# Kernel optimization log

Hardware: AMD Instinct MI355X
Metric: run time of the kernel (lower is better)

The kernel has to match this reference:

```python
import jax, jax.numpy as jnp
import numpy as np

B, V, C, D, H, W = 2, 5, 32, 32, 128, 160


def _grid_sample(img, grid):
    # img: [B,C,H,W]; grid: [B,Hg,Wg,2] in [-1,1]; bilinear, zeros padding, align_corners=True
    Bi, Ci, Hi, Wi = img.shape
    x = (grid[..., 0] + 1.0) * 0.5 * (Wi - 1)
    y = (grid[..., 1] + 1.0) * 0.5 * (Hi - 1)
    x0 = jnp.floor(x); y0 = jnp.floor(y)
    wx = x - x0; wy = y - y0

    def tap(im, ix, iy):
        valid = ((ix >= 0) & (ix <= Wi - 1) & (iy >= 0) & (iy <= Hi - 1)).astype(im.dtype)
        ixc = jnp.clip(ix, 0, Wi - 1).astype(jnp.int32)
        iyc = jnp.clip(iy, 0, Hi - 1).astype(jnp.int32)
        return im[:, iyc, ixc] * valid[None]  # [C,Hg,Wg]

    def one(im, x0b, y0b, wxb, wyb):
        v00 = tap(im, x0b, y0b); v01 = tap(im, x0b + 1, y0b)
        v10 = tap(im, x0b, y0b + 1); v11 = tap(im, x0b + 1, y0b + 1)
        return (v00 * (1 - wxb) + v01 * wxb) * (1 - wyb) + (v10 * (1 - wxb) + v11 * wxb) * wyb

    return jax.vmap(one)(img, x0, y0, wx, wy)


def _homo_warp(src_fea, src_proj, ref_proj, depth_values):
    # src_fea [B,C,H,W], projs [B,4,4], depth_values [B,D,H,W] -> [B,C,D,H,W]
    Bi, Ci, Hi, Wi = src_fea.shape
    Di = depth_values.shape[1]
    proj = src_proj @ jnp.linalg.inv(ref_proj)
    rot, trans = proj[:, :3, :3], proj[:, :3, 3]
    yy, xx = jnp.meshgrid(jnp.arange(Hi, dtype=src_fea.dtype), jnp.arange(Wi, dtype=src_fea.dtype), indexing='ij')
    xyz = jnp.stack([xx.ravel(), yy.ravel(), jnp.ones(Hi * Wi, src_fea.dtype)], 0)  # [3,HW]
    rot_xyz = jnp.einsum('bij,jn->bin', rot, xyz)  # [B,3,HW]
    pxyz = rot_xyz[:, :, None, :] * depth_values.reshape(Bi, 1, Di, Hi * Wi) + trans[:, :, None, None]
    z = pxyz[:, 2]
    gx = (pxyz[:, 0] / z) / ((Wi - 1) / 2) - 1
    gy = (pxyz[:, 1] / z) / ((Hi - 1) / 2) - 1
    grid = jax.lax.stop_gradient(jnp.stack([gx, gy], -1).reshape(Bi, Di * Hi, Wi, 2))  # torch.no_grad block
    return _grid_sample(src_fea, grid).reshape(Bi, Ci, Di, Hi, Wi)


def _pixelwise_net(vol, w0, b0, w1, b1, w2, b2):
    # vol [B,1,D,H,W]; 1x1x1 conv stack + sigmoid + max over depth -> [B,1,H,W]
    x = jax.nn.relu(jnp.einsum('oi,bidhw->bodhw', w0, vol) + b0[None, :, None, None, None])
    x = jax.nn.relu(jnp.einsum('oi,bidhw->bodhw', w1, x) + b1[None, :, None, None, None])
    x = jnp.einsum('oi,bidhw->bodhw', w2, x) + b2[None, :, None, None, None]
    return jnp.max(jax.nn.sigmoid(x), axis=2)


def _cost_reg(vol, w, b):
    out = jax.lax.conv_general_dilated(vol, w, (1, 1, 1), 'SAME', dimension_numbers=('NCDHW', 'OIDHW', 'NCDHW'))
    return out + b[None, :, None, None, None]


def _proj_new(pm):  # pm [B,2,4,4] -> [B,4,4]: K[:3,:3] @ E[:3,:4] into rows 0..2
    top = jnp.einsum('bij,bjk->bik', pm[:, 1, :3, :3], pm[:, 0, :3, :4])
    return pm[:, 0].at[:, :3, :4].set(top)


def _forward(features, proj_matrices, depth_values, pw_w0, pw_b0, pw_w1, pw_b1, pw_w2, pw_b2, reg_w, reg_b):
    proj_new = jax.vmap(_proj_new, in_axes=1, out_axes=1)(proj_matrices)  # [B,V,4,4]
    ref_fea = features[0]
    vol_sum = jnp.zeros((B, 1, D, H, W), features.dtype)  # torch broadcasts [B,1,...] into [B,C,...]; channels identical
    wsum = jnp.full((B, 1, 1, H, W), 1e-5, features.dtype)
    weights = []
    for v in range(1, V):
        warped = _homo_warp(features[v], proj_new[:, v], proj_new[:, 0], depth_values)  # [B,C,D,H,W]
        wvol = jnp.mean(warped * ref_fea[:, :, None], axis=1, keepdims=True)            # [B,1,D,H,W]
        vw = _pixelwise_net(wvol, pw_w0, pw_b0, pw_w1, pw_b1, pw_w2, pw_b2)             # [B,1,H,W]
        weights.append(vw)
        vol_sum = vol_sum + wvol * vw[:, :, None]
        wsum = wsum + vw[:, :, None]
    similarity = jnp.broadcast_to(vol_sum / wsum, (B, C, D, H, W))  # matches torch broadcast-into-C-channel volume
    prob_pre = _cost_reg(similarity, reg_w, reg_b)[:, 0]  # squeeze(1) -> [B,D,H,W]
    prob = jax.nn.softmax(prob_pre, axis=1)
    view_weights = jnp.concatenate(weights, axis=1)  # [B,V-1,H,W]
    idx = jnp.argmax(prob, axis=1, keepdims=True)
    depth = jnp.take_along_axis(depth_values, idx, axis=1)[:, 0]  # WTA depth [B,H,W]
    conf = jnp.max(prob, axis=1)
    return depth, conf, prob, view_weights


def setup_inputs() -> dict:
    key = jax.random.key(0)
    ks = jax.random.split(key, 8)
    features = jax.random.normal(ks[0], (V, B, C, H, W), jnp.float32)
    # Realistic projection matrices: [:,v,0]=extrinsics, [:,v,1,:3,:3]=intrinsics
    Kmat = np.eye(4, dtype=np.float32)
    Kmat[0, 0] = Kmat[1, 1] = 200.0
    Kmat[0, 2] = W / 2.0; Kmat[1, 2] = H / 2.0
    projs = np.zeros((B, V, 2, 4, 4), np.float32)
    for v in range(V):
        E = np.eye(4, dtype=np.float32)
        E[0, 3] = 10.0 * v; E[1, 3] = -5.0 * v  # small baselines
        projs[:, v, 0] = E
        projs[:, v, 1] = Kmat
    proj_matrices = jnp.asarray(projs)
    dv = jnp.linspace(425.0, 935.0, D, dtype=jnp.float32)
    depth_values = jnp.broadcast_to(dv[None, :, None, None], (B, D, H, W))
    def init(k, shape, fan):
        return jax.random.normal(k, shape, jnp.float32) / np.sqrt(fan)
    return {
        'features': features,
        'proj_matrices': proj_matrices,
        'depth_values': depth_values,
        'pw_w0': init(ks[1], (16, 1), 1), 'pw_b0': jnp.zeros(16, jnp.float32),
        'pw_w1': init(ks[2], (8, 16), 16), 'pw_b1': jnp.zeros(8, jnp.float32),
        'pw_w2': init(ks[3], (1, 8), 8), 'pw_b2': jnp.zeros(1, jnp.float32),
        'reg_w': init(ks[4], (1, C, 3, 3, 3), C * 27), 'reg_b': jnp.zeros(1, jnp.float32),
    }


def reference(features, proj_matrices, depth_values, pw_w0, pw_b0, pw_w1, pw_b1, pw_w2, pw_b2, reg_w, reg_b):
    return _forward(features, proj_matrices, depth_values, pw_w0, pw_b0, pw_w1, pw_b1, pw_w2, pw_b2, reg_w, reg_b)
```

## Files before the change

kernel.cpp:

```cpp
#include <hip/hip_runtime.h>
#include <math.h>

#define Bc 2
#define Vc 5
#define Cc 32
#define Dc 32
#define Hc 128
#define Wc 160
#define HWc (Hc*Wc)
#define NSLOT 44
#define TILE_CAP 1024

#define WS_RT     0
#define WS_KW     96
#define FLAG_I    128
#define NS_I      136
#define SHIFT_I   144
#define BBOX_I    856
#define WS_TAPID  912
#define WS_PWL    2960
#define WS_M      3584
#define WS_FEATT  WS_M
#define WS_SIM    (WS_M + 8*NSLOT*HWc)

#define OUT_DEPTH 0
#define OUT_CONF  (Bc*HWc)
#define OUT_PROB  (2*Bc*HWc)
#define OUT_VW    (2*Bc*HWc + Bc*Dc*HWc)

__global__ __launch_bounds__(256) void setup_kernel(
        const float* __restrict__ pm, const float* __restrict__ reg_w,
        const float* __restrict__ dvals,
        const float* __restrict__ w0, const float* __restrict__ b0,
        const float* __restrict__ w1, const float* __restrict__ b1,
        const float* __restrict__ w2, const float* __restrict__ b2,
        float* __restrict__ ws) {
    int t = threadIdx.x;
    int* wsi = (int*)ws;

    if (blockIdx.x == 0) {
        __shared__ float pmL[Bc * Vc * 2 * 16];
        __shared__ int okL[8];

        for (int i = t; i < Bc * Vc * 2 * 16; i += 256) pmL[i] = pm[i];
        if (t >= 32 && t < 32 + 27) {
            int k = t - 32;
            float s = 0.f;
            for (int c = 0; c < Cc; ++c) s += reg_w[c * 27 + k];
            ws[WS_KW + k] = s;
        }
        __syncthreads();

        if (t < Bc * (Vc - 1)) {
            int b = t / (Vc - 1);
            int v = t % (Vc - 1) + 1;
            float dvv[32];
            #pragma unroll
            for (int d = 0; d < Dc; ++d) dvv[d] = dvals[(size_t)(b * Dc + d) * HWc];

            float Pv[16], P0[16];
            for (int which = 0; which < 2; ++which) {
                int vv = which ? 0 : v;
                const float* E = pmL + ((b * Vc + vv) * 2 + 0) * 16;
                const float* K = pmL + ((b * Vc + vv) * 2 + 1) * 16;
                float* P = which ? P0 : Pv;
                for (int i = 0; i < 3; ++i)
                    for (int j = 0; j < 4; ++j) {
                        float s = 0.f;
                        for (int k = 0; k < 3; ++k) s += K[i*4+k] * E[k*4+j];
                        P[i*4+j] = s;
                    }
// ... 64 lines not shown
                    DOTAP(id0, 0, 0)
                    DOTAP(id1, 1, 0)
                    DOTAP(id2, 0, 1)
                    DOTAP(id3, 1, 1)
                    #undef DOTAP
                    #undef GETPREV
                    float4 r0, r1;
                    r0.x = __int_as_float(id0); r0.y = __int_as_float(id1);
                    r0.z = __int_as_float(id2); r0.w = __int_as_float(id3);
                    r1.x = wxv; r1.y = wyv; r1.z = 0.f; r1.w = 0.f;
                    tapOut[d * 2] = r0; tapOut[d * 2 + 1] = r1;
                    pid0 = id0; pid1 = id1; pid2 = id2; pid3 = id3; pix = ix; piy = iy;
                }
                if (n > NSLOT) ok = false;
                if (ok) {
                    for (int s = n; s < NSLOT; ++s) shiftOut[s] = make_int2(sx0, sy0);
                    int dw = 32 + (dxmax - dxmin);
                    int dh = 8 + (dymax - dymin);
                    if (dw * dh > TILE_CAP) ok = false;
                    wsi[BBOX_I + t*4 + 0] = dxmin;
                    wsi[BBOX_I + t*4 + 1] = dymin;
                    wsi[BBOX_I + t*4 + 2] = dw;
                    wsi[BBOX_I + t*4 + 3] = dh;
                }
            }
            okL[t] = ok ? 1 : 0;
            wsi[NS_I + t] = ok ? n : 0;
        }
        __syncthreads();
        if (t == 0) {
            int f = 1;
            for (int i = 0; i < 8; ++i) f &= okL[i];
            wsi[FLAG_I] = f;
            wsi[FLAG_I + 1] = 1;
        }
    } else {
        __shared__ float W0[16], B0[16], W1[128], B1[8], W2[8], B2s;
        __shared__ float rawK[160], t0S[16], sortedS[160];
        __shared__ int nrawS;
        if (t < 16) { W0[t] = w0[t]; B0[t] = b0[t]; }
        if (t < 128) W1[t] = w1[t];
        if (t < 8) { B1[t] = b1[t]; W2[t] = w2[t]; }
        if (t == 0) { B2s = b2[0]; nrawS = 0; }
        __syncthreads();
        if (t < 16 && W0[t] != 0.f) {
            int i = atomicAdd(&nrawS, 1);
            rawK[i] = -B0[t] / W0[t];
        }
        __syncthreads();
        int n0 = nrawS;
        if (t < n0) {
            float v = rawK[t]; int r = 0;
            for (int k = 0; k < n0; ++k) { float o = rawK[k]; r += (o < v) || (o == v && k < t); }
            t0S[r] = v;
        }
        __syncthreads();
        if (t < n0) rawK[t] = t0S[t];
        int nItems = 8 * (n0 + 1);
        if (t < nItems) {
            int j = t / (n0 + 1), m = t % (n0 + 1);
            float se;
            if (n0 == 0) se = 0.f;
            else if (m == 0) se = t0S[0] - 1.f;
            else if (m == n0) se = t0S[n0 - 1] + 1.f;
            else se = 0.5f * (t0S[m - 1] + t0S[m]);
            float aval = B1[j], aslp = 0.f;
            for (int i = 0; i < 16; ++i) {
// ... 8 lines not shown
            }
        }
        __syncthreads();
        int K = nrawS; if (K > 160) K = 160;
        if (t < K) {
            float v = rawK[t]; int r = 0;
            for (int k = 0; k < K; ++k) { float o = rawK[k]; r += (o < v) || (o == v && k < t); }
            sortedS[r] = v;
        }
        __syncthreads();
        ws[WS_PWL + 8 + t] = (t < K) ? sortedS[t] : 1e30f;
        if (t <= K) {
            float se;
            if (K == 0) se = 0.f;
            else if (t == 0) se = sortedS[0] - 1.f;
            else if (t == K) se = sortedS[K - 1] + 1.f;
            else se = 0.5f * (sortedS[t - 1] + sortedS[t]);
            float y = B2s, slp = 0.f;
            for (int j = 0; j < 8; ++j) {
                float aval = B1[j], aslp = 0.f;
                for (int i = 0; i < 16; ++i) {
                    float pre = W0[i] * se + B0[i];
                    if (pre > 0.f) { aval += W1[j * 16 + i] * pre; aslp += W1[j * 16 + i] * W0[i]; }
                }
                if (aval > 0.f) { y += W2[j] * aval; slp += W2[j] * aslp; }
            }
            ws[WS_PWL + 264 + t] = slp;
            ws[WS_PWL + 425 + t] = y - slp * se;
        }
        if (t == 0) ((int*)ws)[WS_PWL] = K;
    }
}

__global__ void check_unif_kernel(const float* __restrict__ dvals, float* __restrict__ ws) {
    int idx = blockIdx.x * 256 + threadIdx.x;
    int plane = idx / HWc;
    float v = dvals[idx];
    if (v != dvals[(size_t)plane * HWc]) ((int*)ws)[FLAG_I + 1] = 0;
}

__global__ __launch_bounds__(256) void mapA_kernel(const float* __restrict__ feat,
                                                   float* __restrict__ ws) {
    const int* wsi = (const int*)ws;
    if (!(wsi[FLAG_I] & wsi[FLAG_I + 1])) return;
    __shared__ float4 tile[TILE_CAP];
    __shared__ int shiftS[NSLOT * 2];
    __shared__ int metaS[4];

    int bv = blockIdx.y;
    int tid = threadIdx.x;
    if (tid < NSLOT * 2) shiftS[tid] = wsi[SHIFT_I + bv * NSLOT * 2 + tid];
    if (tid >= 96 && tid < 100) metaS[tid - 96] = wsi[BBOX_I + bv * 4 + (tid - 96)];
    __syncthreads();

    int ns = wsi[NS_I + bv];
    int dxmin = metaS[0], dymin = metaS[1], dw = metaS[2], dh = metaS[3];
    int ntile = dw * dh;

    int bx = blockIdx.x % (Wc / 32), by = blockIdx.x / (Wc / 32);
    int tx0 = bx * 32, ty0 = by * 8;
    int lx = tid & 31, ly = tid >> 5;
    int p = (ty0 + ly) * Wc + tx0 + lx;

    int b = bv >> 2, vm1 = bv & 3;
    const float* refp = feat + (size_t)b * Cc * HWc + p;
    const float* srcb = feat + (size_t)((vm1 + 1) * Bc + b) * Cc * HWc;

    int soff[NSLOT];
    #pragma unroll
    for (int s = 0; s < NSLOT; ++s)
        soff[s] = (shiftS[2 * s + 1] - dymin) * dw + (shiftS[2 * s] - dxmin);
    int loff = ly * dw + lx;

    float acc[NSLOT];
    #pragma unroll
    for (int s = 0; s < NSLOT; ++s) acc[s] = 0.f;

    for (int g = 0; g < 8; ++g) {
        const float* rp = refp + (size_t)(4 * g) * HWc;
        float r0 = rp[0];
        float r1 = rp[(size_t)HWc];
        float r2 = rp[(size_t)2 * HWc];
        float r3 = rp[(size_t)3 * HWc];
        __syncthreads();
        for (int e = tid; e < ntile; e += 256) {
            int r = e / dw, cc = e - r * dw;
            int gx = tx0 + dxmin + cc, gy = ty0 + dymin + r;
            float4 tv = {0.f, 0.f, 0.f, 0.f};
            if ((unsigned)gx < (unsigned)Wc && (unsigned)gy < (unsigned)Hc) {
                const float* sp = srcb + (size_t)(4 * g) * HWc + gy * Wc + gx;
                tv.x = sp[0];
                tv.y = sp[(size_t)HWc];
                tv.z = sp[(size_t)2 * HWc];
                tv.w = sp[(size_t)3 * HWc];
            }
            tile[e] = tv;
        }
        __syncthreads();
        #pragma unroll
        for (int s = 0; s < NSLOT; ++s) {
            float4 tv = tile[soff[s] + loff];
            acc[s] += r0 * tv.x + r1 * tv.y + r2 * tv.z + r3 * tv.w;
        }
    }

    float* Mout = ws + WS_M + (size_t)bv * NSLOT * HWc + p;
    #pragma unroll
    for (int s = 0; s < NSLOT; ++s)
        if (s < ns) Mout[(size_t)s * HWc] = acc[s] * (1.f / 32.f);
}

__global__ __launch_bounds__(256) void combine_kernel(float* __restrict__ ws,
                                                      float* __restrict__ out) {
    const int* wsi = (const int*)ws;
    if (!(wsi[FLAG_I] & wsi[FLAG_I + 1])) return;
    __shared__ float knotS[256];
    __shared__ float alphaS[161], betaS[161];
    __shared__ float tapS[4 * Dc * 8];
    __shared__ float redS[4][4][64];

    int tid = threadIdx.x;
    int px = tid & 63, oct = tid >> 6;
    int pg = blockIdx.x * 64 + px;
    int b = pg / HWc, p = pg % HWc;

    knotS[tid] = ws[WS_PWL + 8 + tid];
    if (tid < 161) { alphaS[tid] = ws[WS_PWL + 264 + tid]; betaS[tid] = ws[WS_PWL + 425 + tid]; }
    #pragma unroll
    for (int k = 0; k < 4; ++k)
        tapS[tid + k * 256] = ws[WS_TAPID + b * (4 * Dc * 8) + tid + k * 256];
    __syncthreads();

    float vm[4] = {-1e30f, -1e30f, -1e30f, -1e30f};
    for (int dl = 0; dl < 8; ++dl) {
        int d = oct * 8 + dl;
        #pragma unroll
        for (int v = 0; v < 4; ++v) {
            const float* rec = tapS + ((v * Dc + d) << 3);
            int i00 = __float_as_int(rec[0]);
            int i10 = __float_as_int(rec[1]);
            int i01 = __float_as_int(rec[2]);
            int i11 = __float_as_int(rec[3]);
            float wx = rec[4], wy = rec[5];
            const float* Mb = ws + WS_M + ((size_t)(b * 4 + v)) * NSLOT * HWc + p;
            float m00 = Mb[(size_t)i00 * HWc];
            float m10 = Mb[(size_t)i10 * HWc];
            float m01 = Mb[(size_t)i01 * HWc];
            float m11 = Mb[(size_t)i11 * HWc];
            float top = m00 + wx * (m10 - m00);
            float bot = m01 + wx * (m11 - m01);
            float s = top + wy * (bot - top);
            int seg = 0;
            #pragma unroll
            for (int st = 128; st; st >>= 1) {
                int c = seg + st;
                seg = (s >= knotS[c - 1]) ? c : seg;
            }
            float y = fmaf(alphaS[seg], s, betaS[seg]);
            vm[v] = fmaxf(vm[v], y);
        }
    }
    #pragma unroll
    for (int v = 0; v < 4; ++v) redS[oct][v][px] = vm[v];
    __syncthreads();

    float vw[4];
    float wsum = 1e-5f;
    #pragma unroll
    for (int v = 0; v < 4; ++v) {
        float m = fmaxf(fmaxf(redS[0][v][px], redS[1][v][px]),
                        fmaxf(redS[2][v][px], redS[3][v][px]));
        float sig = __fdividef(1.f, 1.f + __expf(-m));
        vw[v] = sig;
        wsum += sig;
    }
    float invw = __fdividef(1.f, wsum);

    for (int dl = 0; dl < 8; ++dl) {
        int d = oct * 8 + dl;
        float vol = 0.f;
        #pragma unroll
        for (int v = 0; v < 4; ++v) {
            const float* rec = tapS + ((v * Dc + d) << 3);
            int i00 = __float_as_int(rec[0]);
            int i10 = __float_as_int(rec[1]);
            int i01 = __float_as_int(rec[2]);
            int i11 = __float_as_int(rec[3]);
            float wx = rec[4], wy = rec[5];
            const float* Mb = ws + WS_M + ((size_t)(b * 4 + v)) * NSLOT * HWc + p;
            float m00 = Mb[(size_t)i00 * HWc];
            float m10 = Mb[(size_t)i10 * HWc];
            float m01 = Mb[(size_t)i01 * HWc];
            float m11 = Mb[(size_t)i11 * HWc];
            float top = m00 + wx * (m10 - m00);
            float bot = m01 + wx * (m11 - m01);
            vol += (top + wy * (bot - top)) * vw[v];
        }
        ws[WS_SIM + ((size_t)(b * Dc + d)) * HWc + p] = vol * invw;
    }
    if (oct == 0) {
        #pragma unroll
        for (int v = 0; v < 4; ++v)
            out[OUT_VW + ((size_t)(b * 4 + v)) * HWc + p] = vw[v];
    }
}

__global__ void transpose_kernel(const float* __restrict__ feat, float* __restrict__ ws) {
    const int* wsi = (const int*)ws;
    if (wsi[FLAG_I] & wsi[FLAG_I + 1]) return;
    __shared__ float tile[32][33];
    int tid = threadIdx.x;
    int total = Vc * Bc * (HWc / 32);
    for (int it = blockIdx.x; it < total; it += gridDim.x) {
        int slab = it / (HWc / 32);
        int pbase = (it % (HWc / 32)) * 32;
        const float* src = feat + (size_t)slab * Cc * HWc;
        float* dst = ws + WS_FEATT + (size_t)slab * HWc * Cc;
        __syncthreads();
        int cc = tid >> 5, pp = tid & 31;
        #pragma unroll
        for (int i = 0; i < 4; ++i) {
            int c = cc + 8 * i;
            tile[c][pp] = src[(size_t)c * HWc + pbase + pp];
        }
        __syncthreads();
        int c2 = tid & 31, p2 = tid >> 5;
        #pragma unroll
        for (int i = 0; i < 4; ++i) {
            int pq = p2 + 8 * i;
            dst[((size_t)(pbase + pq)) * 32 + c2] = tile[c2][pq];
        }
    }
}

__global__ __launch_bounds__(256) void fb_main_kernel(
        const float* __restrict__ dvals,
        const float* __restrict__ w0, const float* __restrict__ b0,
        const float* __restrict__ w1, const float* __restrict__ b1,
        const float* __restrict__ w2, const float* __restrict__ b2,
        float* __restrict__ ws, float* __restrict__ out) {
    const int* wsi = (const int*)ws;
    if (wsi[FLAG_I] & wsi[FLAG_I + 1]) return;
    __shared__ float mlpS[177];
    __shared__ float rtS[96];

    int tid = threadIdx.x;
    if (tid < 16) mlpS[tid] = w0[tid];
    else if (tid < 32) mlpS[tid] = b0[tid - 16];
    else if (tid < 160) mlpS[tid] = w1[tid - 32];
    else if (tid < 168) mlpS[tid] = b1[tid - 160];
    else if (tid < 176) mlpS[tid] = w2[tid - 168];
    else if (tid == 176) mlpS[176] = b2[0];
    if (tid >= 160 && tid < 256 && tid - 160 < 96) rtS[tid - 160] = ws[WS_RT + (tid - 160)];
    __syncthreads();

    int d = tid & 31;
    int pgq = tid >> 5;

    for (int bid = blockIdx.x; bid < Bc * HWc / 8; bid += gridDim.x) {
        int b = bid / (HWc / 8);
        int pblk = (bid % (HWc / 8)) * 8;
        int p = pblk + pgq;
        int h = p / Wc, w = p % Wc;

        const float4* refp = (const float4*)(ws + WS_FEATT + ((size_t)b * HWc + p) * Cc);
        float4 rf[8];
        #pragma unroll
        for (int i = 0; i < 8; ++i) rf[i] = refp[i];

        float depth = dvals[((size_t)(b * Dc + d)) * HWc + p];
        float fx = (float)w, fy = (float)h;

        float sv[4];
        #pragma unroll
        for (int v = 0; v < 4; ++v) {
            const float* rt = rtS + (b * 4 + v) * 12;
            float px = (rt[0] * fx + rt[1] * fy + rt[2]) * depth + rt[9];
            float py = (rt[3] * fx + rt[4] * fy + rt[5]) * depth + rt[10];
            float pz = (rt[6] * fx + rt[7] * fy + rt[8]) * depth + rt[11];
            float xs = __fdividef(px, pz);
            float ys = __fdividef(py, pz);
            float fx0 = floorf(xs), fy0 = floorf(ys);
            float wx = xs - fx0, wy = ys - fy0;

            const float* featv = ws + WS_FEATT + ((size_t)((v + 1) * Bc + b)) * HWc * Cc;
            float acc = 0.f;
            #pragma unroll
            for (int ty = 0; ty < 2; ++ty) {
                #pragma unroll
                for (int tx = 0; tx < 2; ++tx) {
                    float fxt = fx0 + (float)tx;
                    float fyt = fy0 + (float)ty;
                    bool valid = (fxt >= 0.f) && (fxt <= (float)(Wc - 1)) &&
                                 (fyt >= 0.f) && (fyt <= (float)(Hc - 1));
                    float wt = (tx ? wx : 1.f - wx) * (ty ? wy : 1.f - wy);
                    if (valid) {
                        int ix = (int)fxt, iy = (int)fyt;
                        const float4* fp = (const float4*)(featv + ((size_t)iy * Wc + ix) * Cc);
                        float dot = 0.f;
                        #pragma unroll
                        for (int i = 0; i < 8; ++i) {
                            float4 fv = fp[i];
                            dot += fv.x * rf[i].x + fv.y * rf[i].y + fv.z * rf[i].z + fv.w * rf[i].w;
                        }
                        acc += wt * dot;
                    }
                }
            }
            sv[v] = acc * (1.f / (float)Cc);
        }

        float h1[16][4];
        #pragma unroll
        for (int i = 0; i < 16; ++i) {
            float a = mlpS[i], bb = mlpS[16 + i];
            #pragma unroll
            for (int v = 0; v < 4; ++v) h1[i][v] = fmaxf(a * sv[v] + bb, 0.f);
        }
        float bias2 = mlpS[176];
        float y[4] = {bias2, bias2, bias2, bias2};
        const float4* w1v = (const float4*)(mlpS + 32);
        #pragma unroll
        for (int j = 0; j < 8; ++j) {
            float a0 = mlpS[160 + j];
            float acc[4] = {a0, a0, a0, a0};
            #pragma unroll
            for (int k = 0; k < 4; ++k) {
                float4 wq = w1v[j * 4 + k];
                #pragma unroll
                for (int v = 0; v < 4; ++v) {
                    acc[v] += wq.x * h1[4*k+0][v] + wq.y * h1[4*k+1][v]
                            + wq.z * h1[4*k+2][v] + wq.w * h1[4*k+3][v];
                }
            }
            float w2j = mlpS[168 + j];
            #pragma unroll
            for (int v = 0; v < 4; ++v) y[v] += w2j * fmaxf(acc[v], 0.f);
        }

        float vw[4];
        #pragma unroll
        for (int v = 0; v < 4; ++v) {
            float m = __fdividef(1.f, 1.f + __expf(-y[v]));
            #pragma unroll
            for (int off = 16; off; off >>= 1) m = fmaxf(m, __shfl_xor(m, off));
            vw[v] = m;
        }

        float wsum = 1e-5f + vw[0] + vw[1] + vw[2] + vw[3];
        float vol = sv[0] * vw[0] + sv[1] * vw[1] + sv[2] * vw[2] + sv[3] * vw[3];
        ws[WS_SIM + ((size_t)(b * Dc + d)) * HWc + p] = __fdividef(vol, wsum);

        if (d < 4)
            out[OUT_VW + ((size_t)b * 4 + d) * HWc + p] = vw[d];
    }
}

__global__ __launch_bounds__(256) void convsm_kernel(const float* __restrict__ regb,
                                                     const float* __restrict__ dvals,
                                                     const float* __restrict__ ws,
                                                     float* __restrict__ out) {
    __shared__ float pmaxS[32][9];
    __shared__ int   pidxS[32][9];
    __shared__ float psumS[32][9];

    int tid = threadIdx.x;
    int px = tid & 31, q = tid >> 5;
    int p = blockIdx.x * 32 + px;
    int b = blockIdx.y;
    int h = p / Wc, w = p % Wc;

    float kw[27];
    #pragma unroll
    for (int i = 0; i < 27; ++i) kw[i] = ws[WS_KW + i];

    const float* simb = ws + WS_SIM + (size_t)b * Dc * HWc;
    float acc[4] = {0.f, 0.f, 0.f, 0.f};
    #pragma unroll
    for (int e = -1; e <= 4; ++e) {
        int dd = q * 4 + e;
        if (dd < 0 || dd >= Dc) continue;
        float val[3][3];
        #pragma unroll
        for (int i = 0; i < 3; ++i) {
            int hh = h + i - 1;
            #pragma unroll
            for (int j = 0; j < 3; ++j) {
// ... 39 lines not shown

    float sum = 0.f;
    #pragma unroll
    for (int k = 0; k < 8; ++k) sum += psumS[px][k];
    float inv = __fdividef(1.f, sum);

    #pragma unroll
    for (int r = 0; r < 4; ++r)
        out[OUT_PROB + ((size_t)(b * Dc + q * 4 + r)) * HWc + p] =
            ((r == 0) ? e0 : (r == 1) ? e1 : (r == 2) ? e2 : e3) * inv;
    if (q == 0) {
        out[OUT_DEPTH + (size_t)b * HWc + p] = dvals[((size_t)(b * Dc + AM)) * HWc + p];
        out[OUT_CONF + (size_t)b * HWc + p] = inv;
    }
}

extern "C" void kernel_launch(void* const* d_in, const int* in_sizes, int n_in,
                              void* d_out, int out_size, void* d_ws, size_t ws_size,
                              hipStream_t stream) {
    const float* features = (const float*)d_in[0];
    const float* pm       = (const float*)d_in[1];
    const float* dvals    = (const float*)d_in[2];
    const float* pw_w0    = (const float*)d_in[3];
    const float* pw_b0    = (const float*)d_in[4];
    const float* pw_w1    = (const float*)d_in[5];
    const float* pw_b1    = (const float*)d_in[6];
    const float* pw_w2    = (const float*)d_in[7];
    const float* pw_b2    = (const float*)d_in[8];
    const float* reg_w    = (const float*)d_in[9];
    const float* reg_b    = (const float*)d_in[10];
    float* out = (float*)d_out;
    float* ws  = (float*)d_ws;

    setup_kernel<<<2, 256, 0, stream>>>(pm, reg_w, dvals, pw_w0, pw_b0, pw_w1, pw_b1,
                                        pw_w2, pw_b2, ws);
    check_unif_kernel<<<(Bc * Dc * HWc) / 256, 256, 0, stream>>>(dvals, ws);
    transpose_kernel<<<320, 256, 0, stream>>>(features, ws);
    mapA_kernel<<<dim3((Wc / 32) * (Hc / 8), 8), 256, 0, stream>>>(features, ws);
    fb_main_kernel<<<320, 256, 0, stream>>>(dvals, pw_w0, pw_b0, pw_w1, pw_b1,
                                            pw_w2, pw_b2, ws, out);
    combine_kernel<<<Bc * HWc / 64, 256, 0, stream>>>(ws, out);
    convsm_kernel<<<dim3(HWc / 32, Bc), 256, 0, stream>>>(reg_b, dvals, ws, out);
}
```

Before: 80.50 us.

## Merge gated fast/fallback kernels and fold depth-uniformity check into setup

Folds the depth-uniformity check into extra blocks of the setup kernel, using a memset plus an atomicOr flag in place of a separate launch. It pairs the fast-path mapA with the fallback transpose, and the fast-path combine with the fallback main kernel, so that each pair becomes one kernel branching on a gate flag. This cuts the launch count from seven to four plus a memset. The combine path also keeps the interpolated similarities in registers rather than re-gathering them from the workspace in the second pass. The cost is higher register pressure in the merged kernels, and the unused branch's shared-memory allocation may lower occupancy.

```diff
diff --git a/kernel.cpp b/kernel.cpp
--- a/kernel.cpp
+++ b/kernel.cpp
@@ -28,6 +28,8 @@
 #define OUT_PROB  (2*Bc*HWc)
 #define OUT_VW    (2*Bc*HWc + Bc*Dc*HWc)
 
+#define FASTGATE(wsi) (((wsi)[FLAG_I] != 0) && ((wsi)[FLAG_I + 1] == 0))
+
 __global__ __launch_bounds__(256) void setup_kernel(
         const float* __restrict__ pm, const float* __restrict__ reg_w,
         const float* __restrict__ dvals,
@@ -37,6 +39,18 @@
         float* __restrict__ ws) {
     int t = threadIdx.x;
     int* wsi = (int*)ws;
+
+    if (blockIdx.x >= 2) {
+        int nblk = gridDim.x - 2;
+        int stride = nblk * 256;
+        bool bad = false;
+        for (int idx = (blockIdx.x - 2) * 256 + t; idx < Bc * Dc * HWc; idx += stride) {
+            int plane = idx / HWc;
+            if (dvals[idx] != dvals[(size_t)plane * HWc]) bad = true;
+        }
+        if (bad) atomicOr(&wsi[FLAG_I + 1], 1);
+        return;
+    }
 
     if (blockIdx.x == 0) {
         __shared__ float pmL[Bc * Vc * 2 * 16];
@@ -167,7 +181,6 @@
             int f = 1;
             for (int i = 0; i < 8; ++i) f &= okL[i];
             wsi[FLAG_I] = f;
-            wsi[FLAG_I + 1] = 1;
         }
     } else {
         __shared__ float W0[16], B0[16], W1[128], B1[8], W2[8], B2s;
@@ -242,327 +255,302 @@
     }
 }
 
-__global__ void check_unif_kernel(const float* __restrict__ dvals, float* __restrict__ ws) {
-    int idx = blockIdx.x * 256 + threadIdx.x;
-    int plane = idx / HWc;
-    float v = dvals[idx];
-    if (v != dvals[(size_t)plane * HWc]) ((int*)ws)[FLAG_I + 1] = 0;
-}
-
-__global__ __launch_bounds__(256) void mapA_kernel(const float* __restrict__ feat,
-                                                   float* __restrict__ ws) {
+__global__ __launch_bounds__(256) void path1_kernel(const float* __restrict__ feat,
+                                                    float* __restrict__ ws) {
     const int* wsi = (const int*)ws;
-    if (!(wsi[FLAG_I] & wsi[FLAG_I + 1])) return;
-    __shared__ float4 tile[TILE_CAP];
-    __shared__ int shiftS[NSLOT * 2];
-    __shared__ int metaS[4];
-
-    int bv = blockIdx.y;
     int tid = threadIdx.x;
-    if (tid < NSLOT * 2) shiftS[tid] = wsi[SHIFT_I + bv * NSLOT * 2 + tid];
-    if (tid >= 96 && tid < 100) metaS[tid - 96] = wsi[BBOX_I + bv * 4 + (tid - 96)];
-    __syncthreads();
-
-    int ns = wsi[NS_I + bv];
-    int dxmin = metaS[0], dymin = metaS[1], dw = metaS[2], dh = metaS[3];
-    int ntile = dw * dh;
-
-    int bx = blockIdx.x % (Wc / 32), by = blockIdx.x / (Wc / 32);
-    int tx0 = bx * 32, ty0 = by * 8;
-    int lx = tid & 31, ly = tid >> 5;
-    int p = (ty0 + ly) * Wc + tx0 + lx;
-
-    int b = bv >> 2, vm1 = bv & 3;
-    const float* refp = feat + (size_t)b * Cc * HWc + p;
-    const float* srcb = feat + (size_t)((vm1 + 1) * Bc + b) * Cc * HWc;
-
-    int soff[NSLOT];
-    #pragma unroll
-    for (int s = 0; s < NSLOT; ++s)
-        soff[s] = (shiftS[2 * s + 1] - dymin) * dw + (shiftS[2 * s] - dxmin);
-    int loff = ly * dw + lx;
-
-    float acc[NSLOT];
-    #pragma unroll
-    for (int s = 0; s < NSLOT; ++s) acc[s] = 0.f;
-
-    for (int g = 0; g < 8; ++g) {
-        const float* rp = refp + (size_t)(4 * g) * HWc;
-        float r0 = rp[0];
-        float r1 = rp[(size_t)HWc];
-        float r2 = rp[(size_t)2 * HWc];
-        float r3 = rp[(size_t)3 * HWc];
-        __syncthreads();
-        for (int e = tid; e < ntile; e += 256) {
-            int r = e / dw, cc = e - r * dw;
-            int gx = tx0 + dxmin + cc, gy = ty0 + dymin + r;
-            float4 tv = {0.f, 0.f, 0.f, 0.f};
-            if ((unsigned)gx < (unsigned)Wc && (unsigned)gy < (unsigned)Hc) {
-                const float* sp = srcb + (size_t)(4 * g) * HWc + gy * Wc + gx;
-                tv.x = sp[0];
-                tv.y = sp[(size_t)HWc];
-                tv.z = sp[(size_t)2 * HWc];
-                tv.w = sp[(size_t)3 * HWc];
-            }
-            tile[e] = tv;
-        }
-        __syncthreads();
-        #pragma unroll
-        for (int s = 0; s < NSLOT; ++s) {
-            float4 tv = tile[soff[s] + loff];
-            acc[s] += r0 * tv.x + r1 * tv.y + r2 * tv.z + r3 * tv.w;
-        }
-    }
-
-    float* Mout = ws + WS_M + (size_t)bv * NSLOT * HWc + p;
-    #pragma unroll
-    for (int s = 0; s < NSLOT; ++s)
-        if (s < ns) Mout[(size_t)s * HWc] = acc[s] * (1.f / 32.f);
-}
-
-__global__ __launch_bounds__(256) void combine_kernel(float* __restrict__ ws,
-                                                      float* __restrict__ out) {
-    const int* wsi = (const int*)ws;
-    if (!(wsi[FLAG_I] & wsi[FLAG_I + 1])) return;
-    __shared__ float knotS[256];
-    __shared__ float alphaS[161], betaS[161];
-    __shared__ float tapS[4 * Dc * 8];
-    __shared__ float redS[4][4][64];
-
-    int tid = threadIdx.x;
-    int px = tid & 63, oct = tid >> 6;
-    int pg = blockIdx.x * 64 + px;
-    int b = pg / HWc, p = pg % HWc;
-
-    knotS[tid] = ws[WS_PWL + 8 + tid];
-    if (tid < 161) { alphaS[tid] = ws[WS_PWL + 264 + tid]; betaS[tid] = ws[WS_PWL + 425 + tid]; }
-    #pragma unroll
-    for (int k = 0; k < 4; ++k)
-        tapS[tid + k * 256] = ws[WS_TAPID + b * (4 * Dc * 8) + tid + k * 256];
-    __syncthreads();
-
-    float vm[4] = {-1e30f, -1e30f, -1e30f, -1e30f};
-    for (int dl = 0; dl < 8; ++dl) {
-        int d = oct * 8 + dl;
-        #pragma unroll
-        for (int v = 0; v < 4; ++v) {
-            const float* rec = tapS + ((v * Dc + d) << 3);
-            int i00 = __float_as_int(rec[0]);
-            int i10 = __float_as_int(rec[1]);
-            int i01 = __float_as_int(rec[2]);
-            int i11 = __float_as_int(rec[3]);
-            float wx = rec[4], wy = rec[5];
-            const float* Mb = ws + WS_M + ((size_t)(b * 4 + v)) * NSLOT * HWc + p;
-            float m00 = Mb[(size_t)i00 * HWc];
-            float m10 = Mb[(size_t)i10 * HWc];
-            float m01 = Mb[(size_t)i01 * HWc];
-            float m11 = Mb[(size_t)i11 * HWc];
-            float top = m00 + wx * (m10 - m00);
-            float bot = m01 + wx * (m11 - m01);
-            float s = top + wy * (bot - top);
-            int seg = 0;
-            #pragma unroll
-            for (int st = 128; st; st >>= 1) {
-                int c = seg + st;
-                seg = (s >= knotS[c - 1]) ? c : seg;
-            }
-            float y = fmaf(alphaS[seg], s, betaS[seg]);
-            vm[v] = fmaxf(vm[v], y);
-        }
-    }
-    #pragma unroll
-    for (int v = 0; v < 4; ++v) redS[oct][v][px] = vm[v];
-    __syncthreads();
-
-    float vw[4];
-    float wsum = 1e-5f;
-    #pragma unroll
-    for (int v = 0; v < 4; ++v) {
-        float m = fmaxf(fmaxf(redS[0][v][px], redS[1][v][px]),
-                        fmaxf(redS[2][v][px], redS[3][v][px]));
-        float sig = __fdividef(1.f, 1.f + __expf(-m));
-        vw[v] = sig;
-        wsum += sig;
-    }
-    float invw = __fdividef(1.f, wsum);
-
-    for (int dl = 0; dl < 8; ++dl) {
-        int d = oct * 8 + dl;
-        float vol = 0.f;
-        #pragma unroll
-        for (int v = 0; v < 4; ++v) {
-            const float* rec = tapS + ((v * Dc + d) << 3);
-            int i00 = __float_as_int(rec[0]);
-            int i10 = __float_as_int(rec[1]);
-            int i01 = __float_as_int(rec[2]);
-            int i11 = __float_as_int(rec[3]);
-            float wx = rec[4], wy = rec[5];
-            const float* Mb = ws + WS_M + ((size_t)(b * 4 + v)) * NSLOT * HWc + p;
-            float m00 = Mb[(size_t)i00 * HWc];
-            float m10 = Mb[(size_t)i10 * HWc];
-            float m01 = Mb[(size_t)i01 * HWc];
-            float m11 = Mb[(size_t)i11 * HWc];
-            float top = m00 + wx * (m10 - m00);
-            float bot = m01 + wx * (m11 - m01);
-            vol += (top + wy * (bot - top)) * vw[v];
-        }
-        ws[WS_SIM + ((size_t)(b * Dc + d)) * HWc + p] = vol * invw;
-    }
-    if (oct == 0) {
-        #pragma unroll
-        for (int v = 0; v < 4; ++v)
-            out[OUT_VW + ((size_t)(b * 4 + v)) * HWc + p] = vw[v];
+
+    if (FASTGATE(wsi)) {
+        __shared__ float4 tile[TILE_CAP];
+        __shared__ int shiftS[NSLOT * 2];
+        __shared__ int metaS[4];
+
+        int bv = blockIdx.x / 80;
+        int tilei = blockIdx.x % 80;
+        if (tid < NSLOT * 2) shiftS[tid] = wsi[SHIFT_I + bv * NSLOT * 2 + tid];
+        if (tid >= 96 && tid < 100) metaS[tid - 96] = wsi[BBOX_I + bv * 4 + (tid - 96)];
+        __syncthreads();
+
+        int ns = wsi[NS_I + bv];
+        int dxmin = metaS[0], dymin = metaS[1], dw = metaS[2], dh = metaS[3];
+        int ntile = dw * dh;
+
+        int bx = tilei % (Wc / 32), by = tilei / (Wc / 32);
+        int tx0 = bx * 32, ty0 = by * 8;
+        int lx = tid & 31, ly = tid >> 5;
+        int p = (ty0 + ly) * Wc + tx0 + lx;
+
+        int b = bv >> 2, vm1 = bv & 3;
+        const float* refp = feat + (size_t)b * Cc * HWc + p;
+        const float* srcb = feat + (size_t)((vm1 + 1) * Bc + b) * Cc * HWc;
+
+        int soff[NSLOT];
+        #pragma unroll
+        for (int s = 0; s < NSLOT; ++s)
+            soff[s] = (shiftS[2 * s + 1] - dymin) * dw + (shiftS[2 * s] - dxmin);
+        int loff = ly * dw + lx;
+
+        float acc[NSLOT];
+        #pragma unroll
+        for (int s = 0; s < NSLOT; ++s) acc[s] = 0.f;
+
+        for (int g = 0; g < 8; ++g) {
+            const float* rp = refp + (size_t)(4 * g) * HWc;
+            float r0 = rp[0];
+            float r1 = rp[(size_t)HWc];
+            float r2 = rp[(size_t)2 * HWc];
+            float r3 = rp[(size_t)3 * HWc];
+            __syncthreads();
+            for (int e = tid; e < ntile; e += 256) {
+                int r = e / dw, cc = e - r * dw;
+                int gx = tx0 + dxmin + cc, gy = ty0 + dymin + r;
+                float4 tv = {0.f, 0.f, 0.f, 0.f};
+                if ((unsigned)gx < (unsigned)Wc && (unsigned)gy < (unsigned)Hc) {
+                    const float* sp = srcb + (size_t)(4 * g) * HWc + gy * Wc + gx;
+                    tv.x = sp[0];
+                    tv.y = sp[(size_t)HWc];
+                    tv.z = sp[(size_t)2 * HWc];
+                    tv.w = sp[(size_t)3 * HWc];
+                }
+                tile[e] = tv;
+            }
+            __syncthreads();
+            #pragma unroll
+            for (int s = 0; s < NSLOT; ++s) {
+                float4 tv = tile[soff[s] + loff];
+                acc[s] += r0 * tv.x + r1 * tv.y + r2 * tv.z + r3 * tv.w;
+            }
+        }
+
+        float* Mout = ws + WS_M + (size_t)bv * NSLOT * HWc + p;
+        #pragma unroll
+        for (int s = 0; s < NSLOT; ++s)
+            if (s < ns) Mout[(size_t)s * HWc] = acc[s] * (1.f / 32.f);
+    } else {
+        __shared__ float ttile[32][33];
+        int total = Vc * Bc * (HWc / 32);
+        for (int it = blockIdx.x; it < total; it += gridDim.x) {
+            int slab = it / (HWc / 32);
+            int pbase = (it % (HWc / 32)) * 32;
+            const float* src = feat + (size_t)slab * Cc * HWc;
+            float* dst = ws + WS_FEATT + (size_t)slab * HWc * Cc;
+            __syncthreads();
+            int cc = tid >> 5, pp = tid & 31;
+            #pragma unroll
+            for (int i = 0; i < 4; ++i) {
+                int c = cc + 8 * i;
+                ttile[c][pp] = src[(size_t)c * HWc + pbase + pp];
+            }
+            __syncthreads();
+            int c2 = tid & 31, p2 = tid >> 5;
+            #pragma unroll
+            for (int i = 0; i < 4; ++i) {
+                int pq = p2 + 8 * i;
+                dst[((size_t)(pbase + pq)) * 32 + c2] = ttile[c2][pq];
+            }
+        }
     }
 }
 
-__global__ void transpose_kernel(const float* __restrict__ feat, float* __restrict__ ws) {
-    const int* wsi = (const int*)ws;
-    if (wsi[FLAG_I] & wsi[FLAG_I + 1]) return;
-    __shared__ float tile[32][33];
-    int tid = threadIdx.x;
-    int total = Vc * Bc * (HWc / 32);
-    for (int it = blockIdx.x; it < total; it += gridDim.x) {
-        int slab = it / (HWc / 32);
-        int pbase = (it % (HWc / 32)) * 32;
-        const float* src = feat + (size_t)slab * Cc * HWc;
-        float* dst = ws + WS_FEATT + (size_t)slab * HWc * Cc;
-        __syncthreads();
-        int cc = tid >> 5, pp = tid & 31;
-        #pragma unroll
-        for (int i = 0; i < 4; ++i) {
-            int c = cc + 8 * i;
-            tile[c][pp] = src[(size_t)c * HWc + pbase + pp];
-        }
-        __syncthreads();
-        int c2 = tid & 31, p2 = tid >> 5;
-        #pragma unroll
-        for (int i = 0; i < 4; ++i) {
-            int pq = p2 + 8 * i;
-            dst[((size_t)(pbase + pq)) * 32 + c2] = tile[c2][pq];
-        }
-    }
-}
-
-__global__ __launch_bounds__(256) void fb_main_kernel(
+__global__ __launch_bounds__(256) void path2_kernel(
         const float* __restrict__ dvals,
         const float* __restrict__ w0, const float* __restrict__ b0,
         const float* __restrict__ w1, const float* __restrict__ b1,
         const float* __restrict__ w2, const float* __restrict__ b2,
         float* __restrict__ ws, float* __restrict__ out) {
     const int* wsi = (const int*)ws;
-    if (wsi[FLAG_I] & wsi[FLAG_I + 1]) return;
-    __shared__ float mlpS[177];
-    __shared__ float rtS[96];
-
     int tid = threadIdx.x;
-    if (tid < 16) mlpS[tid] = w0[tid];
-    else if (tid < 32) mlpS[tid] = b0[tid - 16];
-    else if (tid < 160) mlpS[tid] = w1[tid - 32];
-    else if (tid < 168) mlpS[tid] = b1[tid - 160];
-    else if (tid < 176) mlpS[tid] = w2[tid - 168];
-    else if (tid == 176) mlpS[176] = b2[0];
-    if (tid >= 160 && tid < 256 && tid - 160 < 96) rtS[tid - 160] = ws[WS_RT + (tid - 160)];
-    __syncthreads();
-
-    int d = tid & 31;
-    int pgq = tid >> 5;
-
-    for (int bid = blockIdx.x; bid < Bc * HWc / 8; bid += gridDim.x) {
-        int b = bid / (HWc / 8);
-        int pblk = (bid % (HWc / 8)) * 8;
-        int p = pblk + pgq;
-        int h = p / Wc, w = p % Wc;
-
-        const float4* refp = (const float4*)(ws + WS_FEATT + ((size_t)b * HWc + p) * Cc);
-        float4 rf[8];
-        #pragma unroll
-        for (int i = 0; i < 8; ++i) rf[i] = refp[i];
-
-        float depth = dvals[((size_t)(b * Dc + d)) * HWc + p];
-        float fx = (float)w, fy = (float)h;
-
-        float sv[4];
+
+    if (FASTGATE(wsi)) {
+        __shared__ float knotS[256];
+        __shared__ float alphaS[161], betaS[161];
+        __shared__ float tapS[4 * Dc * 8];
+        __shared__ float redS[4][4][64];
+
+        int px = tid & 63, oct = tid >> 6;
+        int pg = blockIdx.x * 64 + px;
+        int b = pg / HWc, p = pg % HWc;
+
+        knotS[tid] = ws[WS_PWL + 8 + tid];
+        if (tid < 161) { alphaS[tid] = ws[WS_PWL + 264 + tid]; betaS[tid] = ws[WS_PWL + 425 + tid]; }
+        #pragma unroll
+        for (int k = 0; k < 4; ++k)
+            tapS[tid + k * 256] = ws[WS_TAPID + b * (4 * Dc * 8) + tid + k * 256];
+        __syncthreads();
+
+        float s_arr[8][4];
+        float vm[4] = {-1e30f, -1e30f, -1e30f, -1e30f};
+        #pragma unroll
+        for (int dl = 0; dl < 8; ++dl) {
+            int d = oct * 8 + dl;
+            #pragma unroll
+            for (int v = 0; v < 4; ++v) {
+                const float* rec = tapS + ((v * Dc + d) << 3);
+                int i00 = __float_as_int(rec[0]);
+                int i10 = __float_as_int(rec[1]);
+                int i01 = __float_as_int(rec[2]);
+                int i11 = __float_as_int(rec[3]);
+                float wx = rec[4], wy = rec[5];
+                const float* Mb = ws + WS_M + ((size_t)(b * 4 + v)) * NSLOT * HWc + p;
+                float m00 = Mb[(size_t)i00 * HWc];
+                float m10 = Mb[(size_t)i10 * HWc];
+                float m01 = Mb[(size_t)i01 * HWc];
+                float m11 = Mb[(size_t)i11 * HWc];
+                float top = m00 + wx * (m10 - m00);
+                float bot = m01 + wx * (m11 - m01);
+                float s = top + wy * (bot - top);
+                s_arr[dl][v] = s;
+                int seg = 0;
+                #pragma unroll
+                for (int st = 128; st; st >>= 1) {
+                    int c = seg + st;
+                    seg = (s >= knotS[c - 1]) ? c : seg;
+                }
+                float y = fmaf(alphaS[seg], s, betaS[seg]);
+                vm[v] = fmaxf(vm[v], y);
+            }
+        }
+        #pragma unroll
+        for (int v = 0; v < 4; ++v) redS[oct][v][px] = vm[v];
+        __syncthreads();
+
+        float vw[4];
+        float wsum = 1e-5f;
         #pragma unroll
         for (int v = 0; v < 4; ++v) {
-            const float* rt = rtS + (b * 4 + v) * 12;
-            float px = (rt[0] * fx + rt[1] * fy + rt[2]) * depth + rt[9];
-            float py = (rt[3] * fx + rt[4] * fy + rt[5]) * depth + rt[10];
-            float pz = (rt[6] * fx + rt[7] * fy + rt[8]) * depth + rt[11];
-            float xs = __fdividef(px, pz);
-            float ys = __fdividef(py, pz);
-            float fx0 = floorf(xs), fy0 = floorf(ys);
-            float wx = xs - fx0, wy = ys - fy0;
-
-            const float* featv = ws + WS_FEATT + ((size_t)((v + 1) * Bc + b)) * HWc * Cc;
-            float acc = 0.f;
-            #pragma unroll
-            for (int ty = 0; ty < 2; ++ty) {
-                #pragma unroll
-                for (int tx = 0; tx < 2; ++tx) {
-                    float fxt = fx0 + (float)tx;
-                    float fyt = fy0 + (float)ty;
-                    bool valid = (fxt >= 0.f) && (fxt <= (float)(Wc - 1)) &&
-                                 (fyt >= 0.f) && (fyt <= (float)(Hc - 1));
-                    float wt = (tx ? wx : 1.f - wx) * (ty ? wy : 1.f - wy);
-                    if (valid) {
-                        int ix = (int)fxt, iy = (int)fyt;
-                        const float4* fp = (const float4*)(featv + ((size_t)iy * Wc + ix) * Cc);
-                        float dot = 0.f;
-                        #pragma unroll
-                        for (int i = 0; i < 8; ++i) {
-                            float4 fv = fp[i];
-                            dot += fv.x * rf[i].x + fv.y * rf[i].y + fv.z * rf[i].z + fv.w * rf[i].w;
+            float m = fmaxf(fmaxf(redS[0][v][px], redS[1][v][px]),
+                            fmaxf(redS[2][v][px], redS[3][v][px]));
+            float sig = __fdividef(1.f, 1.f + __expf(-m));
+            vw[v] = sig;
+            wsum += sig;
+        }
+        float invw = __fdividef(1.f, wsum);
+
+        #pragma unroll
+        for (int dl = 0; dl < 8; ++dl) {
+            int d = oct * 8 + dl;
+            float vol = s_arr[dl][0] * vw[0] + s_arr[dl][1] * vw[1]
+                      + s_arr[dl][2] * vw[2] + s_arr[dl][3] * vw[3];
+            ws[WS_SIM + ((size_t)(b * Dc + d)) * HWc + p] = vol * invw;
+        }
+        if (oct == 0) {
+            #pragma unroll
+            for (int v = 0; v < 4; ++v)
+                out[OUT_VW + ((size_t)(b * 4 + v)) * HWc + p] = vw[v];
+        }
+    } else {
+        __shared__ float mlpS[177];
+        __shared__ float rtS[96];
+
+        if (tid < 16) mlpS[tid] = w0[tid];
+        else if (tid < 32) mlpS[tid] = b0[tid - 16];
+        else if (tid < 160) mlpS[tid] = w1[tid - 32];
+        else if (tid < 168) mlpS[tid] = b1[tid - 160];
+        else if (tid < 176) mlpS[tid] = w2[tid - 168];
+        else if (tid == 176) mlpS[176] = b2[0];
+        if (tid >= 160 && tid - 160 < 96) rtS[tid - 160] = ws[WS_RT + (tid - 160)];
+        __syncthreads();
+
+        int d = tid & 31;
+        int pgq = tid >> 5;
+
+        for (int bid = blockIdx.x; bid < Bc * HWc / 8; bid += gridDim.x) {
+            int b = bid / (HWc / 8);
+            int pblk = (bid % (HWc / 8)) * 8;
+            int p = pblk + pgq;
+            int h = p / Wc, w = p % Wc;
+
+            const float4* refp = (const float4*)(ws + WS_FEATT + ((size_t)b * HWc + p) * Cc);
+            float4 rf[8];
+            #pragma unroll
+            for (int i = 0; i < 8; ++i) rf[i] = refp[i];
+
+            float depth = dvals[((size_t)(b * Dc + d)) * HWc + p];
+            float fx = (float)w, fy = (float)h;
+
+            float sv[4];
+            #pragma unroll
+            for (int v = 0; v < 4; ++v) {
+                const float* rt = rtS + (b * 4 + v) * 12;
+                float px = (rt[0] * fx + rt[1] * fy + rt[2]) * depth + rt[9];
+                float py = (rt[3] * fx + rt[4] * fy + rt[5]) * depth + rt[10];
+                float pz = (rt[6] * fx + rt[7] * fy + rt[8]) * depth + rt[11];
+                float xs = __fdividef(px, pz);
+                float ys = __fdividef(py, pz);
+                float fx0 = floorf(xs), fy0 = floorf(ys);
+                float wx = xs - fx0, wy = ys - fy0;
+
+                const float* featv = ws + WS_FEATT + ((size_t)((v + 1) * Bc + b)) * HWc * Cc;
+                float acc = 0.f;
+                #pragma unroll
+                for (int ty = 0; ty < 2; ++ty) {
+                    #pragma unroll
+                    for (int tx = 0; tx < 2; ++tx) {
+                        float fxt = fx0 + (float)tx;
+                        float fyt = fy0 + (float)ty;
+                        bool valid = (fxt >= 0.f) && (fxt <= (float)(Wc - 1)) &&
+                                     (fyt >= 0.f) && (fyt <= (float)(Hc - 1));
+                        float wt = (tx ? wx : 1.f - wx) * (ty ? wy : 1.f - wy);
+                        if (valid) {
+                            int ix = (int)fxt, iy = (int)fyt;
+                            const float4* fp = (const float4*)(featv + ((size_t)iy * Wc + ix) * Cc);
+                            float dot = 0.f;
+                            #pragma unroll
+                            for (int i = 0; i < 8; ++i) {
+                                float4 fv = fp[i];
+                                dot += fv.x * rf[i].x + fv.y * rf[i].y + fv.z * rf[i].z + fv.w * rf[i].w;
+                            }
+                            acc += wt * dot;
                         }
-                        acc += wt * dot;
                     }
                 }
-            }
-            sv[v] = acc * (1.f / (float)Cc);
-        }
-
-        float h1[16][4];
-        #pragma unroll
-        for (int i = 0; i < 16; ++i) {
-            float a = mlpS[i], bb = mlpS[16 + i];
-            #pragma unroll
-            for (int v = 0; v < 4; ++v) h1[i][v] = fmaxf(a * sv[v] + bb, 0.f);
-        }
-        float bias2 = mlpS[176];
-        float y[4] = {bias2, bias2, bias2, bias2};
-        const float4* w1v = (const float4*)(mlpS + 32);
-        #pragma unroll
-        for (int j = 0; j < 8; ++j) {
-            float a0 = mlpS[160 + j];
-            float acc[4] = {a0, a0, a0, a0};
-            #pragma unroll
-            for (int k = 0; k < 4; ++k) {
-                float4 wq = w1v[j * 4 + k];
-                #pragma unroll
-                for (int v = 0; v < 4; ++v) {
-                    acc[v] += wq.x * h1[4*k+0][v] + wq.y * h1[4*k+1][v]
-                            + wq.z * h1[4*k+2][v] + wq.w * h1[4*k+3][v];
-                }
-            }
-            float w2j = mlpS[168 + j];
-            #pragma unroll
-            for (int v = 0; v < 4; ++v) y[v] += w2j * fmaxf(acc[v], 0.f);
-        }
-
-        float vw[4];
-        #pragma unroll
-        for (int v = 0; v < 4; ++v) {
-            float m = __fdividef(1.f, 1.f + __expf(-y[v]));
-            #pragma unroll
-            for (int off = 16; off; off >>= 1) m = fmaxf(m, __shfl_xor(m, off));
-            vw[v] = m;
-        }
-
-        float wsum = 1e-5f + vw[0] + vw[1] + vw[2] + vw[3];
-        float vol = sv[0] * vw[0] + sv[1] * vw[1] + sv[2] * vw[2] + sv[3] * vw[3];
-        ws[WS_SIM + ((size_t)(b * Dc + d)) * HWc + p] = __fdividef(vol, wsum);
-
-        if (d < 4)
-            out[OUT_VW + ((size_t)b * 4 + d) * HWc + p] = vw[d];
+                sv[v] = acc * (1.f / (float)Cc);
+            }
+
+            float h1[16][4];
+            #pragma unroll
+            for (int i = 0; i < 16; ++i) {
+                float a = mlpS[i], bb = mlpS[16 + i];
+                #pragma unroll
+                for (int v = 0; v < 4; ++v) h1[i][v] = fmaxf(a * sv[v] + bb, 0.f);
+            }
+            float bias2 = mlpS[176];
+            float y[4] = {bias2, bias2, bias2, bias2};
+            const float4* w1v = (const float4*)(mlpS + 32);
+            #pragma unroll
+            for (int j = 0; j < 8; ++j) {
+                float a0 = mlpS[160 + j];
+                float acc[4] = {a0, a0, a0, a0};
+                #pragma unroll
+                for (int k = 0; k < 4; ++k) {
+                    float4 wq = w1v[j * 4 + k];
+                    #pragma unroll
+                    for (int v = 0; v < 4; ++v) {
+                        acc[v] += wq.x * h1[4*k+0][v] + wq.y * h1[4*k+1][v]
+                                + wq.z * h1[4*k+2][v] + wq.w * h1[4*k+3][v];
+                    }
+                }
+                float w2j = mlpS[168 + j];
+                #pragma unroll
+                for (int v = 0; v < 4; ++v) y[v] += w2j * fmaxf(acc[v], 0.f);
+            }
+
+            float vw[4];
+            #pragma unroll
+            for (int v = 0; v < 4; ++v) {
+                float m = __fdividef(1.f, 1.f + __expf(-y[v]));
+                #pragma unroll
+                for (int off = 16; off; off >>= 1) m = fmaxf(m, __shfl_xor(m, off));
+                vw[v] = m;
+            }
+
+            float wsum = 1e-5f + vw[0] + vw[1] + vw[2] + vw[3];
+            float vol = sv[0] * vw[0] + sv[1] * vw[1] + sv[2] * vw[2] + sv[3] * vw[3];
+            ws[WS_SIM + ((size_t)(b * Dc + d)) * HWc + p] = __fdividef(vol, wsum);
+
+            if (d < 4)
+                out[OUT_VW + ((size_t)b * 4 + d) * HWc + p] = vw[d];
+        }
     }
 }
 
@@ -668,13 +656,11 @@
     float* out = (float*)d_out;
     float* ws  = (float*)d_ws;
 
-    setup_kernel<<<2, 256, 0, stream>>>(pm, reg_w, dvals, pw_w0, pw_b0, pw_w1, pw_b1,
-                                        pw_w2, pw_b2, ws);
-    check_unif_kernel<<<(Bc * Dc * HWc) / 256, 256, 0, stream>>>(dvals, ws);
-    transpose_kernel<<<320, 256, 0, stream>>>(features, ws);
-    mapA_kernel<<<dim3((Wc / 32) * (Hc / 8), 8), 256, 0, stream>>>(features, ws);
-    fb_main_kernel<<<320, 256, 0, stream>>>(dvals, pw_w0, pw_b0, pw_w1, pw_b1,
-                                            pw_w2, pw_b2, ws, out);
-    combine_kernel<<<Bc * HWc / 64, 256, 0, stream>>>(ws, out);
+    hipMemsetAsync((char*)d_ws + (FLAG_I + 1) * sizeof(int), 0, sizeof(int), stream);
+    setup_kernel<<<130, 256, 0, stream>>>(pm, reg_w, dvals, pw_w0, pw_b0, pw_w1, pw_b1,
+                                          pw_w2, pw_b2, ws);
+    path1_kernel<<<640, 256, 0, stream>>>(features, ws);
+    path2_kernel<<<640, 256, 0, stream>>>(dvals, pw_w0, pw_b0, pw_w1, pw_b1,
+                                          pw_w2, pw_b2, ws, out);
     convsm_kernel<<<dim3(HWc / 32, Bc), 256, 0, stream>>>(reg_b, dvals, ws, out);
 }
```

After: 89.26 us. 10.9% more time.

## Fold depth-uniformity check into setup kernel and drop feature transpose

Applied to the files above, without the earlier changes.

Moves the per-element depth-uniformity check into extra blocks of the setup kernel, which set a non-uniform flag through atomicOr after a memset clears it. This removes one kernel launch. It also drops the transpose kernel: the fallback path now reads features directly in channel-major layout with strided loads instead of the transposed copy. The launch count on the fast path shrinks, but the fallback gather becomes uncoalesced, and correctness now depends on the memset and the inverted flag meaning.

```diff
diff --git a/kernel.cpp b/kernel.cpp
--- a/kernel.cpp
+++ b/kernel.cpp
@@ -20,13 +20,14 @@
 #define WS_TAPID  912
 #define WS_PWL    2960
 #define WS_M      3584
-#define WS_FEATT  WS_M
 #define WS_SIM    (WS_M + 8*NSLOT*HWc)
 
 #define OUT_DEPTH 0
 #define OUT_CONF  (Bc*HWc)
 #define OUT_PROB  (2*Bc*HWc)
 #define OUT_VW    (2*Bc*HWc + Bc*Dc*HWc)
+
+#define IS_FAST(wsi) (((wsi)[FLAG_I] != 0) && ((wsi)[FLAG_I + 1] == 0))
 
 __global__ __launch_bounds__(256) void setup_kernel(
         const float* __restrict__ pm, const float* __restrict__ reg_w,
@@ -37,6 +38,17 @@
         float* __restrict__ ws) {
     int t = threadIdx.x;
     int* wsi = (int*)ws;
+
+    if (blockIdx.x >= 2) {
+        int stride = (gridDim.x - 2) * 256;
+        bool bad = false;
+        for (int idx = (blockIdx.x - 2) * 256 + t; idx < Bc * Dc * HWc; idx += stride) {
+            int plane = idx / HWc;
+            if (dvals[idx] != dvals[(size_t)plane * HWc]) bad = true;
+        }
+        if (bad) atomicOr(&wsi[FLAG_I + 1], 1);
+        return;
+    }
 
     if (blockIdx.x == 0) {
         __shared__ float pmL[Bc * Vc * 2 * 16];
@@ -167,7 +179,6 @@
             int f = 1;
             for (int i = 0; i < 8; ++i) f &= okL[i];
             wsi[FLAG_I] = f;
-            wsi[FLAG_I + 1] = 1;
         }
     } else {
         __shared__ float W0[16], B0[16], W1[128], B1[8], W2[8], B2s;
@@ -242,17 +253,10 @@
     }
 }
 
-__global__ void check_unif_kernel(const float* __restrict__ dvals, float* __restrict__ ws) {
-    int idx = blockIdx.x * 256 + threadIdx.x;
-    int plane = idx / HWc;
-    float v = dvals[idx];
-    if (v != dvals[(size_t)plane * HWc]) ((int*)ws)[FLAG_I + 1] = 0;
-}
-
 __global__ __launch_bounds__(256) void mapA_kernel(const float* __restrict__ feat,
                                                    float* __restrict__ ws) {
     const int* wsi = (const int*)ws;
-    if (!(wsi[FLAG_I] & wsi[FLAG_I + 1])) return;
+    if (!IS_FAST(wsi)) return;
     __shared__ float4 tile[TILE_CAP];
     __shared__ int shiftS[NSLOT * 2];
     __shared__ int metaS[4];
@@ -323,7 +327,7 @@
 __global__ __launch_bounds__(256) void combine_kernel(float* __restrict__ ws,
                                                       float* __restrict__ out) {
     const int* wsi = (const int*)ws;
-    if (!(wsi[FLAG_I] & wsi[FLAG_I + 1])) return;
+    if (!IS_FAST(wsi)) return;
     __shared__ float knotS[256];
     __shared__ float alphaS[161], betaS[161];
     __shared__ float tapS[4 * Dc * 8];
@@ -415,42 +419,14 @@
     }
 }
 
-__global__ void transpose_kernel(const float* __restrict__ feat, float* __restrict__ ws) {
-    const int* wsi = (const int*)ws;
-    if (wsi[FLAG_I] & wsi[FLAG_I + 1]) return;
-    __shared__ float tile[32][33];
-    int tid = threadIdx.x;
-    int total = Vc * Bc * (HWc / 32);
-    for (int it = blockIdx.x; it < total; it += gridDim.x) {
-        int slab = it / (HWc / 32);
-        int pbase = (it % (HWc / 32)) * 32;
-        const float* src = feat + (size_t)slab * Cc * HWc;
-        float* dst = ws + WS_FEATT + (size_t)slab * HWc * Cc;
-        __syncthreads();
-        int cc = tid >> 5, pp = tid & 31;
-        #pragma unroll
-        for (int i = 0; i < 4; ++i) {
-            int c = cc + 8 * i;
-            tile[c][pp] = src[(size_t)c * HWc + pbase + pp];
-        }
-        __syncthreads();
-        int c2 = tid & 31, p2 = tid >> 5;
-        #pragma unroll
-        for (int i = 0; i < 4; ++i) {
-            int pq = p2 + 8 * i;
-            dst[((size_t)(pbase + pq)) * 32 + c2] = tile[c2][pq];
-        }
-    }
-}
-
 __global__ __launch_bounds__(256) void fb_main_kernel(
-        const float* __restrict__ dvals,
+        const float* __restrict__ feat, const float* __restrict__ dvals,
         const float* __restrict__ w0, const float* __restrict__ b0,
         const float* __restrict__ w1, const float* __restrict__ b1,
         const float* __restrict__ w2, const float* __restrict__ b2,
         float* __restrict__ ws, float* __restrict__ out) {
     const int* wsi = (const int*)ws;
-    if (wsi[FLAG_I] & wsi[FLAG_I + 1]) return;
+    if (IS_FAST(wsi)) return;
     __shared__ float mlpS[177];
     __shared__ float rtS[96];
 
@@ -473,10 +449,10 @@
         int p = pblk + pgq;
         int h = p / Wc, w = p % Wc;
 
-        const float4* refp = (const float4*)(ws + WS_FEATT + ((size_t)b * HWc + p) * Cc);
-        float4 rf[8];
-        #pragma unroll
-        for (int i = 0; i < 8; ++i) rf[i] = refp[i];
+        const float* refb = feat + (size_t)b * Cc * HWc + p;
+        float rf[Cc];
+        #pragma unroll
+        for (int c = 0; c < Cc; ++c) rf[c] = refb[(size_t)c * HWc];
 
         float depth = dvals[((size_t)(b * Dc + d)) * HWc + p];
         float fx = (float)w, fy = (float)h;
@@ -493,7 +469,7 @@
             float fx0 = floorf(xs), fy0 = floorf(ys);
             float wx = xs - fx0, wy = ys - fy0;
 
-            const float* featv = ws + WS_FEATT + ((size_t)((v + 1) * Bc + b)) * HWc * Cc;
+            const float* featv = feat + (size_t)((v + 1) * Bc + b) * Cc * HWc;
             float acc = 0.f;
             #pragma unroll
             for (int ty = 0; ty < 2; ++ty) {
@@ -506,13 +482,11 @@
                     float wt = (tx ? wx : 1.f - wx) * (ty ? wy : 1.f - wy);
                     if (valid) {
                         int ix = (int)fxt, iy = (int)fyt;
-                        const float4* fp = (const float4*)(featv + ((size_t)iy * Wc + ix) * Cc);
+                        const float* fp = featv + (size_t)(iy * Wc + ix);
                         float dot = 0.f;
                         #pragma unroll
-                        for (int i = 0; i < 8; ++i) {
-                            float4 fv = fp[i];
-                            dot += fv.x * rf[i].x + fv.y * rf[i].y + fv.z * rf[i].z + fv.w * rf[i].w;
-                        }
+                        for (int c = 0; c < Cc; ++c)
+                            dot += rf[c] * fp[(size_t)c * HWc];
                         acc += wt * dot;
                     }
                 }
@@ -668,12 +642,11 @@
     float* out = (float*)d_out;
     float* ws  = (float*)d_ws;
 
-    setup_kernel<<<2, 256, 0, stream>>>(pm, reg_w, dvals, pw_w0, pw_b0, pw_w1, pw_b1,
-                                        pw_w2, pw_b2, ws);
-    check_unif_kernel<<<(Bc * Dc * HWc) / 256, 256, 0, stream>>>(dvals, ws);
-    transpose_kernel<<<320, 256, 0, stream>>>(features, ws);
+    hipMemsetAsync((char*)d_ws + (FLAG_I + 1) * sizeof(int), 0, sizeof(int), stream);
+    setup_kernel<<<130, 256, 0, stream>>>(pm, reg_w, dvals, pw_w0, pw_b0, pw_w1, pw_b1,
+                                          pw_w2, pw_b2, ws);
     mapA_kernel<<<dim3((Wc / 32) * (Hc / 8), 8), 256, 0, stream>>>(features, ws);
-    fb_main_kernel<<<320, 256, 0, stream>>>(dvals, pw_w0, pw_b0, pw_w1, pw_b1,
+    fb_main_kernel<<<320, 256, 0, stream>>>(features, dvals, pw_w0, pw_b0, pw_w1, pw_b1,
                                             pw_w2, pw_b2, ws, out);
     combine_kernel<<<Bc * HWc / 64, 256, 0, stream>>>(ws, out);
     convsm_kernel<<<dim3(HWc / 32, Bc), 256, 0, stream>>>(reg_b, dvals, ws, out);
```

Result: no change. 79.37 us (-1.4%).
